# Performance work log

Measured on AMD Instinct MI355X. Metric: run time of the kernel, lower is better.

## Reference

```python
import jax, jax.numpy as jnp
import numpy as np

SQ, SK, B, H, D = 2048, 2048, 2, 16, 64
LAYER_NUMBER = 1  # coeff for query_key_layer_scaling
MASK_FILL = -10000.0  # attention_mask_func fill value


def setup_inputs() -> dict:
    key = jax.random.key(0)
    kq, kk, kv = jax.random.split(key, 3)
    query_layer = jax.random.normal(kq, (SQ, B, H, D), dtype=jnp.float32)
    key_layer = jax.random.normal(kk, (SK, B, H, D), dtype=jnp.float32)
    value_layer = jax.random.normal(kv, (SK, B, H, D), dtype=jnp.float32)
    attention_mask = jnp.zeros((B, 1, SQ, SK), dtype=bool)  # ignored for causal mask type
    return {
        "query_layer": query_layer,
        "key_layer": key_layer,
        "value_layer": value_layer,
        "attention_mask": attention_mask,
    }


def reference(query_layer, key_layer, value_layer, attention_mask):
    sq, b, h, d = query_layer.shape
    sk = key_layer.shape[0]
    coeff = float(LAYER_NUMBER)
    norm_factor = np.sqrt(d) * coeff  # norm_factor = sqrt(d) * layer_number

    # BMM1: [b,h,sq,sk] scores, scaled by 1/norm_factor
    scores = jnp.einsum("sbhd,tbhd->bhst", query_layer, key_layer) / norm_factor

    # FusedScaleMaskSoftmax: scale by coeff in fp32, causal mask, softmax
    scores = scores.astype(jnp.float32) * coeff
    causal = jnp.triu(jnp.ones((sq, sk), dtype=bool), k=1)  # True above diagonal -> masked
    scores = jnp.where(causal[None, None], MASK_FILL, scores)
    probs = jax.nn.softmax(scores, axis=-1).astype(query_layer.dtype)

    # dropout p=0.0 -> identity

    # BMM2: context [sq,b,h,d] -> [sq,b,h*d]
    context = jnp.einsum("bhst,tbhd->sbhd", probs, value_layer)
    return context.reshape(sq, b, h * d)
```

## Files before the change

kernel.cpp:

```cpp
#include <hip/hip_runtime.h>

typedef short bf16x8 __attribute__((ext_vector_type(8)));
typedef float f32x4 __attribute__((ext_vector_type(4)));
typedef unsigned u32x4 __attribute__((ext_vector_type(4)));
typedef unsigned u32x2 __attribute__((ext_vector_type(2)));
typedef unsigned short ushort_t;

#define RS 2048
#define LDSK 72
#define QSCALE 0.18033688011f
#define BH_STRIDE (2048*64)

static __device__ __forceinline__ unsigned pkbf(float a, float b) {
    union { float f; unsigned u; } ua, ub; ua.f = a; ub.f = b;
    return ((ua.u + 0x8000u) >> 16) | ((ub.u + 0x8000u) & 0xffff0000u);
}

static __device__ __forceinline__ float fexp2(float x) {
#if __has_builtin(__builtin_amdgcn_exp2f)
    return __builtin_amdgcn_exp2f(x);
#else
    return exp2f(x);
#endif
}

__global__ __launch_bounds__(256)
void prep_bf16(const float* __restrict__ K, const float* __restrict__ V,
               ushort_t* __restrict__ Kbf, ushort_t* __restrict__ Vtb)
{
    __shared__ short Tt[64 * LDSK];
    const int kt = blockIdx.x, bh = blockIdx.y;
    const int t = threadIdx.x;

    {
        const int key = t >> 2, cq = (t & 3) * 16;
        const float* kp = K + (size_t)(kt * 64 + key) * RS + bh * 64 + cq;
        f32x4 a0 = *(const f32x4*)kp,     a1 = *(const f32x4*)(kp + 4);
        f32x4 a2 = *(const f32x4*)(kp + 8), a3 = *(const f32x4*)(kp + 12);
        u32x4 w0, w1;
        w0[0] = pkbf(a0[0], a0[1]); w0[1] = pkbf(a0[2], a0[3]);
        w0[2] = pkbf(a1[0], a1[1]); w0[3] = pkbf(a1[2], a1[3]);
        w1[0] = pkbf(a2[0], a2[1]); w1[1] = pkbf(a2[2], a2[3]);
        w1[2] = pkbf(a3[0], a3[1]); w1[3] = pkbf(a3[2], a3[3]);
        ushort_t* kout = Kbf + (size_t)bh * BH_STRIDE + (size_t)(kt * 64 + key) * 64 + cq;
        *(u32x4*)kout = w0;
        *(u32x4*)(kout + 8) = w1;
    }
    {
        const int vkey = (t & 31) * 2, vd = (t >> 5) * 8;
        const float* vp = V + (size_t)(kt * 64 + vkey) * RS + bh * 64 + vd;
        f32x4 b0 = *(const f32x4*)vp,        b1 = *(const f32x4*)(vp + 4);
        f32x4 c0 = *(const f32x4*)(vp + RS), c1 = *(const f32x4*)(vp + RS + 4);
        #pragma unroll
        for (int i = 0; i < 4; ++i) {
            *(unsigned*)&Tt[(vd + i) * LDSK + vkey]     = pkbf(b0[i], c0[i]);
            *(unsigned*)&Tt[(vd + 4 + i) * LDSK + vkey] = pkbf(b1[i], c1[i]);
        }
    }
    __syncthreads();
    {
        const int d = t >> 2, kq = (t & 3) * 16;
        ushort_t* vout = Vtb + (size_t)bh * BH_STRIDE + (size_t)d * RS + kt * 64 + kq;
        u32x4 w0 = *(const u32x4*)&Tt[d * LDSK + kq];
        u32x4 w1 = *(const u32x4*)&Tt[d * LDSK + kq + 8];
        *(u32x4*)vout = w0;
        *(u32x4*)(vout + 8) = w1;
    }
}

__global__ __launch_bounds__(256, 4)
void fa_fwd2(const float* __restrict__ Q, const ushort_t* __restrict__ Kbf,
             const ushort_t* __restrict__ Vtb, float* __restrict__ Out)
{
    __shared__ short Ksh[64 * LDSK];
    __shared__ short Vt[64 * LDSK];
    __shared__ short Psh[4][16 * LDSK];

    const int x = blockIdx.x;
    const int chunk = x >> 8, idx = x & 255;
    const int bh = idx & 31, s = idx >> 5;
    const int qt = (chunk == 0) ? (31 - s) : (chunk == 1) ? (23 - s)
                 : (chunk == 2) ? s : (8 + s);
    const int base = bh * 64;
    const int tid = threadIdx.x;
    const int wave = tid >> 6, lane = tid & 63;
    const int n15 = lane & 15, quad = lane >> 4;
    const int q0 = qt * 64;

    const int r0 = tid >> 3, cc = (tid & 7) * 8;
    const ushort_t* kb = Kbf + (size_t)bh * BH_STRIDE + r0 * 64 + cc;
    const ushort_t* vb = Vtb + (size_t)bh * BH_STRIDE + (size_t)r0 * RS + cc;

    bf16x8 qf[2];
    {
        const float* qp = Q + (size_t)(q0 + wave * 16 + n15) * RS + base + quad * 8;
        #pragma unroll
        for (int ks = 0; ks < 2; ++ks) {
            f32x4 a0 = *(const f32x4*)(qp + ks * 32) * QSCALE;
            f32x4 a1 = *(const f32x4*)(qp + ks * 32 + 4) * QSCALE;
            union { u32x4 u; bf16x8 s; } w;
            w.u[0] = pkbf(a0[0], a0[1]); w.u[1] = pkbf(a0[2], a0[3]);
            w.u[2] = pkbf(a1[0], a1[1]); w.u[3] = pkbf(a1[2], a1[3]);
            qf[ks] = w.s;
        }
    }

    f32x4 O[4];
    #pragma unroll
    for (int i = 0; i < 4; ++i) O[i] = (f32x4){0.f, 0.f, 0.f, 0.f};
    float l = 0.f;

    u32x4 pk0, pk1, pv0, pv1;
    auto prefetch = [&](int kt) {
        const ushort_t* kp = kb + (size_t)kt * 4096;
        pk0 = *(const u32x4*)kp;
        pk1 = *(const u32x4*)(kp + 32 * 64);
        const ushort_t* vp = vb + kt * 64;
        pv0 = *(const u32x4*)vp;
        pv1 = *(const u32x4*)(vp + 32 * RS);
    };
    auto stage = [&]() {
        *(u32x4*)&Ksh[r0 * LDSK + cc] = pk0;
        *(u32x4*)&Ksh[(r0 + 32) * LDSK + cc] = pk1;
        *(u32x4*)&Vt[r0 * LDSK + cc] = pv0;
        *(u32x4*)&Vt[(r0 + 32) * LDSK + cc] = pv1;
    };

    auto compute = [&](int kb_, bool diag) {
        f32x4 S[4];
        #pragma unroll
        for (int mb = 0; mb < 4; ++mb) {
            f32x4 sv = (f32x4){0.f, 0.f, 0.f, 0.f};
            bf16x8 kf0 = *(const bf16x8*)&Ksh[(mb * 16 + n15) * LDSK + quad * 8];
            sv = __builtin_amdgcn_mfma_f32_16x16x32_bf16(kf0, qf[0], sv, 0, 0, 0);
            bf16x8 kf1 = *(const bf16x8*)&Ksh[(mb * 16 + n15) * LDSK + 32 + quad * 8];
            sv = __builtin_amdgcn_mfma_f32_16x16x32_bf16(kf1, qf[1], sv, 0, 0, 0);
            S[mb] = sv;
        }
        if (diag) {
            int q = q0 + wave * 16 + n15;
            #pragma unroll
            for (int mb = 0; mb < 4; ++mb)
                #pragma unroll
                for (int r = 0; r < 4; ++r)
                    if (kb_ + mb * 16 + quad * 4 + r > q) S[mb][r] = -1e30f;
        }
        float rs = 0.f;
        #pragma unroll
        for (int mb = 0; mb < 4; ++mb) {
            float p0 = fexp2(S[mb][0]), p1 = fexp2(S[mb][1]);
            float p2 = fexp2(S[mb][2]), p3 = fexp2(S[mb][3]);
            rs += (p0 + p1) + (p2 + p3);
            u32x2 w; w[0] = pkbf(p0, p1); w[1] = pkbf(p2, p3);
            *(u32x2*)&Psh[wave][n15 * LDSK + mb * 16 + quad * 4] = w;
        }
        rs += __shfl_xor(rs, 16);
        rs += __shfl_xor(rs, 32);
        l += rs;
        bf16x8 pf0 = *(const bf16x8*)&Psh[wave][n15 * LDSK + quad * 8];
        bf16x8 pf1 = *(const bf16x8*)&Psh[wave][n15 * LDSK + 32 + quad * 8];
        #pragma unroll
        for (int db = 0; db < 4; ++db) {
            bf16x8 vf0 = *(const bf16x8*)&Vt[(db * 16 + n15) * LDSK + quad * 8];
            O[db] = __builtin_amdgcn_mfma_f32_16x16x32_bf16(pf0, vf0, O[db], 0, 0, 0);
            bf16x8 vf1 = *(const bf16x8*)&Vt[(db * 16 + n15) * LDSK + 32 + quad * 8];
            O[db] = __builtin_amdgcn_mfma_f32_16x16x32_bf16(pf1, vf1, O[db], 0, 0, 0);
        }
    };

    prefetch(0);
    for (int kt = 0; kt <= qt; ++kt) {
        __syncthreads();
        stage();
        __syncthreads();
        if (kt < qt) prefetch(kt + 1);
        compute(kt * 64, kt == qt);
    }

    #pragma unroll
    for (int r = 0; r < 4; ++r) {
        float inv = 1.0f / __shfl(l, quad * 4 + r);
        size_t row = (size_t)(q0 + wave * 16 + quad * 4 + r) * RS + base;
        #pragma unroll
        for (int db = 0; db < 4; ++db)
            Out[row + db * 16 + n15] = O[db][r] * inv;
    }
}

__global__ __launch_bounds__(256, 3)
void fa_fwd_fb(const float* __restrict__ Q, const float* __restrict__ K,
               const float* __restrict__ V, float* __restrict__ Out)
{
    __shared__ short Ksh[2][64 * LDSK];
    __shared__ short Vt[2][64 * LDSK];
    __shared__ short Psh[4][16 * LDSK];

    const int qt = 31 - blockIdx.y;
    const int bh = blockIdx.x;
    const int base = bh * 64;
    const int tid = threadIdx.x;
    const int wave = tid >> 6, lane = tid & 63;
    const int n15 = lane & 15, quad = lane >> 4;
    const int q0 = qt * 64;
    const int krow = tid >> 2, kcg = (tid & 3) * 16;
    const int vkey = (tid & 31) * 2, vd = (tid >> 5) * 4;

    bf16x8 qf[2];
    {
        const float* qp = Q + (size_t)(q0 + wave * 16 + n15) * RS + base + quad * 8;
        #pragma unroll
        for (int ks = 0; ks < 2; ++ks) {
            f32x4 a0 = *(const f32x4*)(qp + ks * 32) * QSCALE;
            f32x4 a1 = *(const f32x4*)(qp + ks * 32 + 4) * QSCALE;
            union { u32x4 u; bf16x8 s; } w;
            w.u[0] = pkbf(a0[0], a0[1]); w.u[1] = pkbf(a0[2], a0[3]);
            w.u[2] = pkbf(a1[0], a1[1]); w.u[3] = pkbf(a1[2], a1[3]);
            qf[ks] = w.s;
        }
    }
    f32x4 O[4];
    #pragma unroll
    for (int i = 0; i < 4; ++i) O[i] = (f32x4){0.f, 0.f, 0.f, 0.f};
    float l = 0.f;
    f32x4 rk0, rk1, rk2, rk3, rv0, rv1, rv2, rv3;
    auto prefetch = [&](int kt) {
        const int kb = kt * 64;
        const float* kp = K + (size_t)(kb + krow) * RS + base + kcg;
        rk0 = *(const f32x4*)kp;       rk1 = *(const f32x4*)(kp + 4);
        rk2 = *(const f32x4*)(kp + 8); rk3 = *(const f32x4*)(kp + 12);
        const float* vp = V + (size_t)(kb + vkey) * RS + base + vd;
        rv0 = *(const f32x4*)vp;        rv1 = *(const f32x4*)(vp + RS);
        rv2 = *(const f32x4*)(vp + 32); rv3 = *(const f32x4*)(vp + RS + 32);
    };
    auto stage = [&](int buf) {
        u32x4 w0; w0[0] = pkbf(rk0[0], rk0[1]); w0[1] = pkbf(rk0[2], rk0[3]);
                  w0[2] = pkbf(rk1[0], rk1[1]); w0[3] = pkbf(rk1[2], rk1[3]);
        *(u32x4*)&Ksh[buf][krow * LDSK + kcg] = w0;
        u32x4 w1; w1[0] = pkbf(rk2[0], rk2[1]); w1[1] = pkbf(rk2[2], rk2[3]);
                  w1[2] = pkbf(rk3[0], rk3[1]); w1[3] = pkbf(rk3[2], rk3[3]);
        *(u32x4*)&Ksh[buf][krow * LDSK + kcg + 8] = w1;
        #pragma unroll
        for (int i = 0; i < 4; ++i) {
            *(unsigned*)&Vt[buf][(vd + i) * LDSK + vkey] = pkbf(rv0[i], rv1[i]);
            *(unsigned*)&Vt[buf][(vd + 32 + i) * LDSK + vkey] = pkbf(rv2[i], rv3[i]);
        }
    };
    auto compute = [&](int buf, int kb, bool diag) {
        f32x4 S[4];
        #pragma unroll
        for (int mb = 0; mb < 4; ++mb) {
            f32x4 sv = (f32x4){0.f, 0.f, 0.f, 0.f};
            bf16x8 kf0 = *(const bf16x8*)&Ksh[buf][(mb * 16 + n15) * LDSK + quad * 8];
            sv = __builtin_amdgcn_mfma_f32_16x16x32_bf16(kf0, qf[0], sv, 0, 0, 0);
            bf16x8 kf1 = *(const bf16x8*)&Ksh[buf][(mb * 16 + n15) * LDSK + 32 + quad * 8];
            sv = __builtin_amdgcn_mfma_f32_16x16x32_bf16(kf1, qf[1], sv, 0, 0, 0);
            S[mb] = sv;
        }
        if (diag) {
            int q = q0 + wave * 16 + n15;
            #pragma unroll
            for (int mb = 0; mb < 4; ++mb)
                #pragma unroll
                for (int r = 0; r < 4; ++r)
                    if (kb + mb * 16 + quad * 4 + r > q) S[mb][r] = -1e30f;
        }
        float rs = 0.f;
        #pragma unroll
        for (int mb = 0; mb < 4; ++mb) {
            float p0 = fexp2(S[mb][0]), p1 = fexp2(S[mb][1]);
            float p2 = fexp2(S[mb][2]), p3 = fexp2(S[mb][3]);
            rs += (p0 + p1) + (p2 + p3);
            u32x2 w; w[0] = pkbf(p0, p1); w[1] = pkbf(p2, p3);
            *(u32x2*)&Psh[wave][n15 * LDSK + mb * 16 + quad * 4] = w;
        }
        rs += __shfl_xor(rs, 16);
        rs += __shfl_xor(rs, 32);
        l += rs;
        bf16x8 pf0 = *(const bf16x8*)&Psh[wave][n15 * LDSK + quad * 8];
        bf16x8 pf1 = *(const bf16x8*)&Psh[wave][n15 * LDSK + 32 + quad * 8];
        #pragma unroll
        for (int db = 0; db < 4; ++db) {
            bf16x8 vf0 = *(const bf16x8*)&Vt[buf][(db * 16 + n15) * LDSK + quad * 8];
            O[db] = __builtin_amdgcn_mfma_f32_16x16x32_bf16(pf0, vf0, O[db], 0, 0, 0);
            bf16x8 vf1 = *(const bf16x8*)&Vt[buf][(db * 16 + n15) * LDSK + 32 + quad * 8];
            O[db] = __builtin_amdgcn_mfma_f32_16x16x32_bf16(pf1, vf1, O[db], 0, 0, 0);
        }
    };
    prefetch(0);
    stage(0);
    __syncthreads();
    for (int kt = 0; kt <= qt; ++kt) {
        const int cur = kt & 1;
        if (kt < qt) prefetch(kt + 1);
        compute(cur, kt * 64, kt == qt);
        if (kt < qt) stage(1 - cur);
        __syncthreads();
    }
    #pragma unroll
    for (int r = 0; r < 4; ++r) {
        float inv = 1.0f / __shfl(l, quad * 4 + r);
        size_t row = (size_t)(q0 + wave * 16 + quad * 4 + r) * RS + base;
        #pragma unroll
        for (int db = 0; db < 4; ++db)
            Out[row + db * 16 + n15] = O[db][r] * inv;
    }
}

extern "C" void kernel_launch(void* const* d_in, const int* in_sizes, int n_in,
                              void* d_out, int out_size, void* d_ws, size_t ws_size,
                              hipStream_t stream) {
    const float* Q = (const float*)d_in[0];
    const float* K = (const float*)d_in[1];
    const float* V = (const float*)d_in[2];
    float* Out = (float*)d_out;

    if (ws_size >= (size_t)2 * 32 * BH_STRIDE * sizeof(ushort_t)) {
        ushort_t* Kbf = (ushort_t*)d_ws;
        ushort_t* Vtb = Kbf + (size_t)32 * BH_STRIDE;
        prep_bf16<<<dim3(32, 32), dim3(256), 0, stream>>>(K, V, Kbf, Vtb);
        fa_fwd2<<<dim3(1024), dim3(256), 0, stream>>>(Q, Kbf, Vtb, Out);
    } else {
        fa_fwd_fb<<<dim3(32, 32), dim3(256), 0, stream>>>(Q, K, V, Out);
    }
}
```

Baseline: 138.5 us.

## Double-buffer K/V via direct global-to-LDS loads with XOR-swizzled layout

Replaces the register-staged K/V prefetch, which used two barriers per tile, with double-buffered LDS tiles filled by global_load_lds DMA. One barrier per iteration overlaps the next tile's load with compute. The LDS layout changes from padded rows to an XOR swizzle to avoid bank conflicts, and the P buffer shrinks to a half-width stride that is staged in two halves. It also adds hardware bf16 pack conversion and s_setprio around the MFMA blocks. This raises LDS use and relies on correct vmcnt handling for the async LDS writes.

```diff
diff --git a/kernel.cpp b/kernel.cpp
--- a/kernel.cpp
+++ b/kernel.cpp
@@ -8,6 +8,7 @@
 
 #define RS 2048
 #define LDSK 72
+#define PSTR 40
 #define QSCALE 0.18033688011f
 #define BH_STRIDE (2048*64)
 
@@ -22,6 +23,12 @@
 #else
     return exp2f(x);
 #endif
+}
+
+static __device__ __forceinline__ void gload16(const ushort_t* g, short* l) {
+    __builtin_amdgcn_global_load_lds(
+        (const __attribute__((address_space(1))) unsigned int*)(g),
+        (__attribute__((address_space(3))) unsigned int*)(l), 16, 0, 0);
 }
 
 __global__ __launch_bounds__(256)
@@ -69,12 +76,12 @@
 }
 
 __global__ __launch_bounds__(256, 4)
-void fa_fwd2(const float* __restrict__ Q, const ushort_t* __restrict__ Kbf,
+void fa_fwd3(const float* __restrict__ Q, const ushort_t* __restrict__ Kbf,
              const ushort_t* __restrict__ Vtb, float* __restrict__ Out)
 {
-    __shared__ short Ksh[64 * LDSK];
-    __shared__ short Vt[64 * LDSK];
-    __shared__ short Psh[4][16 * LDSK];
+    __shared__ alignas(16) short Kd[2][4096];
+    __shared__ alignas(16) short Vd[2][4096];
+    __shared__ alignas(16) short Psh[4][16 * PSTR];
 
     const int x = blockIdx.x;
     const int chunk = x >> 8, idx = x & 255;
@@ -83,13 +90,26 @@
                  : (chunk == 2) ? s : (8 + s);
     const int base = bh * 64;
     const int tid = threadIdx.x;
-    const int wave = tid >> 6, lane = tid & 63;
-    const int n15 = lane & 15, quad = lane >> 4;
+    const int wave = tid >> 6;
+    const int n15 = tid & 15, quad = (tid & 63) >> 4;
     const int q0 = qt * 64;
 
-    const int r0 = tid >> 3, cc = (tid & 7) * 8;
-    const ushort_t* kb = Kbf + (size_t)bh * BH_STRIDE + r0 * 64 + cc;
-    const ushort_t* vb = Vtb + (size_t)bh * BH_STRIDE + (size_t)r0 * RS + cc;
+    const int srow = tid >> 3, sg = (tid & 7) ^ (srow & 7);
+    const ushort_t* kb2 = Kbf + (size_t)bh * BH_STRIDE + srow * 64 + sg * 8;
+    const ushort_t* vb2 = Vtb + (size_t)bh * BH_STRIDE + (size_t)srow * RS + sg * 8;
+
+    auto stage = [&](int buf, int kt) {
+        const ushort_t* ks = kb2 + (size_t)kt * 4096;
+        const ushort_t* vs = vb2 + kt * 64;
+        short* kd = &Kd[buf][wave * 512];
+        short* vd = &Vd[buf][wave * 512];
+        gload16(ks,         kd);
+        gload16(ks + 2048,  kd + 2048);
+        gload16(vs,         vd);
+        gload16(vs + 65536, vd + 2048);
+    };
+
+    stage(0, 0);
 
     bf16x8 qf[2];
     {
@@ -110,71 +130,82 @@
     for (int i = 0; i < 4; ++i) O[i] = (f32x4){0.f, 0.f, 0.f, 0.f};
     float l = 0.f;
 
-    u32x4 pk0, pk1, pv0, pv1;
-    auto prefetch = [&](int kt) {
-        const ushort_t* kp = kb + (size_t)kt * 4096;
-        pk0 = *(const u32x4*)kp;
-        pk1 = *(const u32x4*)(kp + 32 * 64);
-        const ushort_t* vp = vb + kt * 64;
-        pv0 = *(const u32x4*)vp;
-        pv1 = *(const u32x4*)(vp + 32 * RS);
-    };
-    auto stage = [&]() {
-        *(u32x4*)&Ksh[r0 * LDSK + cc] = pk0;
-        *(u32x4*)&Ksh[(r0 + 32) * LDSK + cc] = pk1;
-        *(u32x4*)&Vt[r0 * LDSK + cc] = pv0;
-        *(u32x4*)&Vt[(r0 + 32) * LDSK + cc] = pv1;
-    };
-
-    auto compute = [&](int kb_, bool diag) {
+    const int c0 = (quad * 8) ^ ((n15 & 7) * 8);
+    const int c1 = c0 ^ 32;
+
+    asm volatile("s_waitcnt vmcnt(0)" ::: "memory");
+    __builtin_amdgcn_sched_barrier(0);
+    __builtin_amdgcn_s_barrier();
+
+    int buf = 0;
+    for (int kt = 0; kt <= qt; ++kt) {
+        if (kt < qt) stage(buf ^ 1, kt + 1);
+        const short* Kb_ = Kd[buf];
+        const short* Vb_ = Vd[buf];
+
         f32x4 S[4];
+        __builtin_amdgcn_s_setprio(1);
         #pragma unroll
         for (int mb = 0; mb < 4; ++mb) {
+            const short* kr = Kb_ + (mb * 16 + n15) * 64;
+            bf16x8 kf0 = *(const bf16x8*)(kr + c0);
+            bf16x8 kf1 = *(const bf16x8*)(kr + c1);
             f32x4 sv = (f32x4){0.f, 0.f, 0.f, 0.f};
-            bf16x8 kf0 = *(const bf16x8*)&Ksh[(mb * 16 + n15) * LDSK + quad * 8];
             sv = __builtin_amdgcn_mfma_f32_16x16x32_bf16(kf0, qf[0], sv, 0, 0, 0);
-            bf16x8 kf1 = *(const bf16x8*)&Ksh[(mb * 16 + n15) * LDSK + 32 + quad * 8];
             sv = __builtin_amdgcn_mfma_f32_16x16x32_bf16(kf1, qf[1], sv, 0, 0, 0);
             S[mb] = sv;
         }
-        if (diag) {
-            int q = q0 + wave * 16 + n15;
+        __builtin_amdgcn_s_setprio(0);
+
+        if (kt == qt) {
+            const int kb_ = kt * 64;
+            const int q = q0 + wave * 16 + n15;
             #pragma unroll
             for (int mb = 0; mb < 4; ++mb)
                 #pragma unroll
                 for (int r = 0; r < 4; ++r)
                     if (kb_ + mb * 16 + quad * 4 + r > q) S[mb][r] = -1e30f;
         }
+
         float rs = 0.f;
-        #pragma unroll
-        for (int mb = 0; mb < 4; ++mb) {
-            float p0 = fexp2(S[mb][0]), p1 = fexp2(S[mb][1]);
-            float p2 = fexp2(S[mb][2]), p3 = fexp2(S[mb][3]);
-            rs += (p0 + p1) + (p2 + p3);
-            u32x2 w; w[0] = pkbf(p0, p1); w[1] = pkbf(p2, p3);
-            *(u32x2*)&Psh[wave][n15 * LDSK + mb * 16 + quad * 4] = w;
+        bf16x8 pf[2];
+        #pragma unroll
+        for (int half = 0; half < 2; ++half) {
+            #pragma unroll
+            for (int m2 = 0; m2 < 2; ++m2) {
+                f32x4 sv = S[half * 2 + m2];
+                float p0 = fexp2(sv[0]), p1 = fexp2(sv[1]);
+                float p2 = fexp2(sv[2]), p3 = fexp2(sv[3]);
+                rs += (p0 + p1) + (p2 + p3);
+                unsigned w0, w1;
+                asm("v_cvt_pk_bf16_f32 %0, %1, %2" : "=v"(w0) : "v"(p0), "v"(p1));
+                asm("v_cvt_pk_bf16_f32 %0, %1, %2" : "=v"(w1) : "v"(p2), "v"(p3));
+                u32x2 w; w[0] = w0; w[1] = w1;
+                *(u32x2*)&Psh[wave][n15 * PSTR + m2 * 16 + quad * 4] = w;
+            }
+            pf[half] = *(const bf16x8*)&Psh[wave][n15 * PSTR + quad * 8];
         }
         rs += __shfl_xor(rs, 16);
         rs += __shfl_xor(rs, 32);
         l += rs;
-        bf16x8 pf0 = *(const bf16x8*)&Psh[wave][n15 * LDSK + quad * 8];
-        bf16x8 pf1 = *(const bf16x8*)&Psh[wave][n15 * LDSK + 32 + quad * 8];
+
+        __builtin_amdgcn_s_setprio(1);
         #pragma unroll
         for (int db = 0; db < 4; ++db) {
-            bf16x8 vf0 = *(const bf16x8*)&Vt[(db * 16 + n15) * LDSK + quad * 8];
-            O[db] = __builtin_amdgcn_mfma_f32_16x16x32_bf16(pf0, vf0, O[db], 0, 0, 0);
-            bf16x8 vf1 = *(const bf16x8*)&Vt[(db * 16 + n15) * LDSK + 32 + quad * 8];
-            O[db] = __builtin_amdgcn_mfma_f32_16x16x32_bf16(pf1, vf1, O[db], 0, 0, 0);
-        }
-    };
-
-    prefetch(0);
-    for (int kt = 0; kt <= qt; ++kt) {
-        __syncthreads();
-        stage();
-        __syncthreads();
-        if (kt < qt) prefetch(kt + 1);
-        compute(kt * 64, kt == qt);
+            const short* vr = Vb_ + (db * 16 + n15) * 64;
+            bf16x8 vf0 = *(const bf16x8*)(vr + c0);
+            O[db] = __builtin_amdgcn_mfma_f32_16x16x32_bf16(pf[0], vf0, O[db], 0, 0, 0);
+            bf16x8 vf1 = *(const bf16x8*)(vr + c1);
+            O[db] = __builtin_amdgcn_mfma_f32_16x16x32_bf16(pf[1], vf1, O[db], 0, 0, 0);
+        }
+        __builtin_amdgcn_s_setprio(0);
+
+        if (kt < qt) {
+            asm volatile("s_waitcnt vmcnt(0)" ::: "memory");
+            __builtin_amdgcn_sched_barrier(0);
+            __builtin_amdgcn_s_barrier();
+            buf ^= 1;
+        }
     }
 
     #pragma unroll
@@ -318,7 +349,7 @@
         ushort_t* Kbf = (ushort_t*)d_ws;
         ushort_t* Vtb = Kbf + (size_t)32 * BH_STRIDE;
         prep_bf16<<<dim3(32, 32), dim3(256), 0, stream>>>(K, V, Kbf, Vtb);
-        fa_fwd2<<<dim3(1024), dim3(256), 0, stream>>>(Q, Kbf, Vtb, Out);
+        fa_fwd3<<<dim3(1024), dim3(256), 0, stream>>>(Q, Kbf, Vtb, Out);
     } else {
         fa_fwd_fb<<<dim3(32, 32), dim3(256), 0, stream>>>(Q, K, V, Out);
     }
```

After: 141.2 us (median of 2 runs). No clear change (+2.0%).
